# Performance work log

Hardware: AMD Instinct MI355X
Metric: run time of the kernel (lower is better)

## Reference

```python
import jax, jax.numpy as jnp
import numpy as np

B = 1024          # number of graphs in batch
NUM_NODES = 360   # ROIs per graph (max nodes in dense batch)
NUM_HEADS = 8
D_FEAT = 256


def to_dense_batch(x, batch, num_graphs, max_nodes):
    """Scatter ragged node features [total, d] into dense [num_graphs, max_nodes, d].
    Assumes `batch` is sorted (as torch_geometric's to_dense_batch does)."""
    total = x.shape[0]
    counts = jax.ops.segment_sum(jnp.ones(total, jnp.int32), batch,
                                 num_segments=num_graphs)
    starts = jnp.concatenate([jnp.zeros(1, jnp.int32),
                              jnp.cumsum(counts)[:-1].astype(jnp.int32)])
    pos = jnp.arange(total) - starts[batch]           # intra-graph position
    flat_idx = batch * max_nodes + pos                # index into padded buffer
    dense = jnp.zeros((num_graphs * max_nodes, x.shape[1]), x.dtype)
    dense = dense.at[flat_idx].set(x)
    return dense.reshape(num_graphs, max_nodes, x.shape[1])


def setup_inputs() -> dict:
    key = jax.random.key(0)
    k1, k2 = jax.random.split(key)
    x = jax.random.normal(k1, (B * NUM_NODES, D_FEAT), dtype=jnp.float32)
    batch = jnp.repeat(jnp.arange(B, dtype=jnp.int64), NUM_NODES)
    w = jax.random.uniform(k2, (NUM_NODES, NUM_HEADS), dtype=jnp.float32)
    return {"x": x, "batch": batch, "w": w}


def reference(x, batch, w):
    dense = to_dense_batch(x, batch, B, NUM_NODES)        # [B, N, d]
    attn = jax.nn.softmax(w, axis=0)                      # softmax over nodes, [N, H]
    pooled = jnp.einsum('bnd,nh->bhd', dense, attn)       # == (x^T @ sm(w))^T
    return pooled.reshape(B, NUM_HEADS * D_FEAT)          # [B, H*d]
```

## Files before the change

### kernel.cpp

```cpp
#include <hip/hip_runtime.h>

#define B_GRAPHS 1024
#define NN 360
#define HH 8
#define DD 256
#define D4 64

__global__ __launch_bounds__(256, 4) void roigp_fused_kernel(
        const float4* __restrict__ x,
        const float*  __restrict__ w,
        float4* __restrict__ out) {
    __shared__ __align__(16) char smem[4 * HH * D4 * 16];
    float* s_attn = (float*)smem;
    float4 (*s_red)[HH][D4] = (float4 (*)[HH][D4])smem;

    const int b    = blockIdx.x;
    const int lane = threadIdx.x & 63;
    const int wave = threadIdx.x >> 6;

    #pragma unroll
    for (int h = wave; h < HH; h += 4) {
        float m = -1e30f;
        for (int n = lane; n < NN; n += 64) m = fmaxf(m, w[n * HH + h]);
        #pragma unroll
        for (int off = 32; off > 0; off >>= 1) m = fmaxf(m, __shfl_xor(m, off));

        float s = 0.f;
        for (int n = lane; n < NN; n += 64) s += __expf(w[n * HH + h] - m);
        #pragma unroll
        for (int off = 32; off > 0; off >>= 1) s += __shfl_xor(s, off);

        const float inv = 1.f / s;
        for (int n = lane; n < NN; n += 64)
            s_attn[n * HH + h] = __expf(w[n * HH + h] - m) * inv;
    }
    __syncthreads();

    const float4* xb = x + (size_t)b * NN * D4 + lane;

    float4 acc[HH];
    #pragma unroll
    for (int h = 0; h < HH; ++h) acc[h] = make_float4(0.f, 0.f, 0.f, 0.f);

    #pragma unroll 5
    for (int n = wave; n < NN; n += 4) {
        const float4 xv = xb[(size_t)n * D4];
        const float4 a0 = ((const float4*)(s_attn + n * HH))[0];
        const float4 a1 = ((const float4*)(s_attn + n * HH))[1];
        const float av[8] = {a0.x, a0.y, a0.z, a0.w, a1.x, a1.y, a1.z, a1.w};
        #pragma unroll
        for (int h = 0; h < HH; ++h) {
            acc[h].x = fmaf(xv.x, av[h], acc[h].x);
            acc[h].y = fmaf(xv.y, av[h], acc[h].y);
            acc[h].z = fmaf(xv.z, av[h], acc[h].z);
            acc[h].w = fmaf(xv.w, av[h], acc[h].w);
        }
    }

    __syncthreads();
    #pragma unroll
    for (int h = 0; h < HH; ++h) s_red[wave][h][lane] = acc[h];
    __syncthreads();

    #pragma unroll
    for (int s = threadIdx.x; s < HH * D4; s += 256) {
        const int h = s >> 6, l = s & 63;
        const float4 r0 = s_red[0][h][l];
        const float4 r1 = s_red[1][h][l];
        const float4 r2 = s_red[2][h][l];
        const float4 r3 = s_red[3][h][l];
        float4 o;
        o.x = r0.x + r1.x + r2.x + r3.x;
        o.y = r0.y + r1.y + r2.y + r3.y;
        o.z = r0.z + r1.z + r2.z + r3.z;
        o.w = r0.w + r1.w + r2.w + r3.w;
        out[(size_t)b * (HH * D4) + s] = o;
    }
}

extern "C" void kernel_launch(void* const* d_in, const int* in_sizes, int n_in,
                              void* d_out, int out_size, void* d_ws, size_t ws_size,
                              hipStream_t stream) {
    const float* x = (const float*)d_in[0];
    const float* w = (const float*)d_in[2];

    roigp_fused_kernel<<<B_GRAPHS, 256, 0, stream>>>(
        (const float4*)x, w, (float4*)d_out);
}
```

Before: 509.5 us.

## Hoist softmax into separate kernel and give each wave a contiguous row slab

Softmax over w is now computed once by a single-block kernel into workspace, and the main kernel copies the precomputed attention into LDS instead of recomputing it in every block. Each wave processes a contiguous range of 90 rows, loading 6 rows at a time into registers before the FMAs to increase memory-level parallelism. This adds a second kernel launch and a dependency between the two kernels.

```diff
diff --git a/kernel.cpp b/kernel.cpp
--- a/kernel.cpp
+++ b/kernel.cpp
@@ -5,16 +5,11 @@
 #define HH 8
 #define DD 256
 #define D4 64
+#define ROWS_PER_WAVE 90
+#define CHUNK 6
 
-__global__ __launch_bounds__(256, 4) void roigp_fused_kernel(
-        const float4* __restrict__ x,
-        const float*  __restrict__ w,
-        float4* __restrict__ out) {
-    __shared__ __align__(16) char smem[4 * HH * D4 * 16];
-    float* s_attn = (float*)smem;
-    float4 (*s_red)[HH][D4] = (float4 (*)[HH][D4])smem;
-
-    const int b    = blockIdx.x;
+__global__ __launch_bounds__(256) void roigp_softmax_kernel(
+        const float* __restrict__ w, float* __restrict__ attn) {
     const int lane = threadIdx.x & 63;
     const int wave = threadIdx.x >> 6;
 
@@ -32,28 +27,56 @@
 
         const float inv = 1.f / s;
         for (int n = lane; n < NN; n += 64)
-            s_attn[n * HH + h] = __expf(w[n * HH + h] - m) * inv;
+            attn[n * HH + h] = __expf(w[n * HH + h] - m) * inv;
     }
+}
+
+__global__ __launch_bounds__(256, 4) void roigp_fused_kernel(
+        const float4* __restrict__ x,
+        const float4* __restrict__ attn4,
+        float4* __restrict__ out) {
+    __shared__ __align__(16) char smem[4 * HH * D4 * 16];
+    float* s_attn = (float*)smem;
+    float4 (*s_red)[HH][D4] = (float4 (*)[HH][D4])smem;
+
+    const int b    = blockIdx.x;
+    const int lane = threadIdx.x & 63;
+    const int wave = threadIdx.x >> 6;
+
+    float4* s_attn4 = (float4*)s_attn;
+    #pragma unroll
+    for (int i = threadIdx.x; i < NN * HH / 4; i += 256)
+        s_attn4[i] = attn4[i];
     __syncthreads();
 
-    const float4* xb = x + (size_t)b * NN * D4 + lane;
+    const int n0 = wave * ROWS_PER_WAVE;
+    const float4* __restrict__ xp = x + ((size_t)b * NN + n0) * D4 + lane;
 
     float4 acc[HH];
     #pragma unroll
     for (int h = 0; h < HH; ++h) acc[h] = make_float4(0.f, 0.f, 0.f, 0.f);
 
-    #pragma unroll 5
-    for (int n = wave; n < NN; n += 4) {
-        const float4 xv = xb[(size_t)n * D4];
-        const float4 a0 = ((const float4*)(s_attn + n * HH))[0];
-        const float4 a1 = ((const float4*)(s_attn + n * HH))[1];
-        const float av[8] = {a0.x, a0.y, a0.z, a0.w, a1.x, a1.y, a1.z, a1.w};
+    #pragma unroll 1
+    for (int c = 0; c < ROWS_PER_WAVE / CHUNK; ++c) {
+        float4 xq[CHUNK];
         #pragma unroll
-        for (int h = 0; h < HH; ++h) {
-            acc[h].x = fmaf(xv.x, av[h], acc[h].x);
-            acc[h].y = fmaf(xv.y, av[h], acc[h].y);
-            acc[h].z = fmaf(xv.z, av[h], acc[h].z);
-            acc[h].w = fmaf(xv.w, av[h], acc[h].w);
+        for (int j = 0; j < CHUNK; ++j)
+            xq[j] = xp[(size_t)(c * CHUNK + j) * D4];
+
+        #pragma unroll
+        for (int j = 0; j < CHUNK; ++j) {
+            const float4 xv = xq[j];
+            const float* ap = s_attn + (n0 + c * CHUNK + j) * HH;
+            const float4 a0 = *(const float4*)ap;
+            const float4 a1 = *(const float4*)(ap + 4);
+#define FMA4(A, S) \
+            A.x = fmaf(xv.x, S, A.x); A.y = fmaf(xv.y, S, A.y); \
+            A.z = fmaf(xv.z, S, A.z); A.w = fmaf(xv.w, S, A.w);
+            FMA4(acc[0], a0.x) FMA4(acc[1], a0.y)
+            FMA4(acc[2], a0.z) FMA4(acc[3], a0.w)
+            FMA4(acc[4], a1.x) FMA4(acc[5], a1.y)
+            FMA4(acc[6], a1.z) FMA4(acc[7], a1.w)
+#undef FMA4
         }
     }
 
@@ -83,7 +106,9 @@
                               hipStream_t stream) {
     const float* x = (const float*)d_in[0];
     const float* w = (const float*)d_in[2];
+    float* attn = (float*)d_ws;
 
+    roigp_softmax_kernel<<<1, 256, 0, stream>>>(w, attn);
     roigp_fused_kernel<<<B_GRAPHS, 256, 0, stream>>>(
-        (const float4*)x, w, (float4*)d_out);
+        (const float4*)x, (const float4*)attn, (float4*)d_out);
 }
```

Measured after the change: 503.3 us. Within noise of the previous version (-1.2%).
